# Performance work log

Measured on AMD Instinct MI355X. Metric: run time of the kernel, lower is better.

## Reference

```python
import jax, jax.numpy as jnp
import numpy as np

N_NODES = 50000
N_EDGES = 800000
D = 128
N_LAYERS = 4


def _sage_conv(x, edge_index, Wl, bl, Wr):
    # PyG SAGEConv (mean aggr): out = lin_l(mean_{j in N(i)} x_j) + lin_r(x_i)
    src, dst = edge_index[0], edge_index[1]
    msgs = x[src]                                            # [E, D] gather
    summed = jax.ops.segment_sum(msgs, dst, num_segments=N_NODES)   # [N, D]
    cnt = jax.ops.segment_sum(jnp.ones((msgs.shape[0],), x.dtype), dst,
                              num_segments=N_NODES)
    mean = summed / jnp.maximum(cnt, 1.0)[:, None]           # [N, D]
    return mean @ Wl.T + bl + x @ Wr.T


def setup_inputs() -> dict:
    key = jax.random.key(0)
    ks = jax.random.split(key, 2 + 3 * N_LAYERS)
    x = jax.random.normal(ks[0], (N_NODES, D), dtype=jnp.float32)
    edge_index = jax.random.randint(ks[1], (2, N_EDGES), 0, N_NODES, dtype=jnp.int64)
    inp = {"x": x, "edge_index": edge_index}
    s = 1.0 / np.sqrt(D)
    for i in range(N_LAYERS):
        inp[f"Wl{i}"] = jax.random.uniform(ks[2 + 3 * i], (D, D), jnp.float32, -s, s)
        inp[f"bl{i}"] = jax.random.uniform(ks[3 + 3 * i], (D,), jnp.float32, -s, s)
        inp[f"Wr{i}"] = jax.random.uniform(ks[4 + 3 * i], (D, D), jnp.float32, -s, s)
    return inp


def reference(x, edge_index, Wl0, bl0, Wr0, Wl1, bl1, Wr1, Wl2, bl2, Wr2, Wl3, bl3, Wr3):
    # ReLU only after the first conv, per the original forward.
    h = jax.nn.relu(_sage_conv(x, edge_index, Wl0, bl0, Wr0))
    h = _sage_conv(h, edge_index, Wl1, bl1, Wr1)
    h = _sage_conv(h, edge_index, Wl2, bl2, Wr2)
    h = _sage_conv(h, edge_index, Wl3, bl3, Wr3)
    return h
```

## Files before the change

### kernel.cpp

```cpp
#include <hip/hip_runtime.h>
#include <stdint.h>

#define NN 50000
#define NE 800000
#define CAST_B 6250
#define CVTW_B 512
#define EPB 8192
#define HIST_B 98
#define NBK 196
#define FUSE_B 782

typedef short short8 __attribute__((ext_vector_type(8)));
typedef float f32x4 __attribute__((ext_vector_type(4)));
typedef unsigned int uint;
typedef unsigned short ushort;

__device__ __forceinline__ uint rne_bf16(float f) {
    uint x = __float_as_uint(f);
    return (x + 0x7FFFu + ((x >> 16) & 1u)) >> 16;
}
__device__ __forceinline__ float bf_lo(uint d) { return __uint_as_float(d << 16); }
__device__ __forceinline__ float bf_hi(uint d) { return __uint_as_float(d & 0xFFFF0000u); }

__device__ __forceinline__ int ei_is64(const int* __restrict__ ei) {
    return (ei[1] | ei[3] | ei[5] | ei[7]) == 0;
}

struct Ptrs8 { const float* p[8]; };

__global__ __launch_bounds__(256) void k_prep(
    const float* __restrict__ x, ushort* __restrict__ xbf, Ptrs8 ps,
    ushort* __restrict__ wbf, const int* __restrict__ ei,
    uint* __restrict__ ebuf, int* __restrict__ hcnt) {
    __shared__ int hs[NBK];
    int b = blockIdx.x;
    if (b < CAST_B) {
        int i = b * 256 + threadIdx.x;
        float4 v = ((const float4*)x)[i];
        uint2 o;
        o.x = rne_bf16(v.x) | (rne_bf16(v.y) << 16);
        o.y = rne_bf16(v.z) | (rne_bf16(v.w) << 16);
        ((uint2*)xbf)[i] = o;
    } else if (b < CAST_B + CVTW_B) {
        int idx = (b - CAST_B) * 256 + threadIdx.x;
        int m = idx >> 14;
        int o14 = idx & 16383;
        int k0i = (o14 >> 12) & 3;
        int t = (o14 >> 9) & 7;
        int lane6 = (o14 >> 3) & 63;
        int e = o14 & 7;
        int r = t * 16 + (lane6 & 15);
        int c = k0i * 32 + (lane6 >> 4) * 8 + e;
        wbf[idx] = (ushort)rne_bf16(ps.p[m][r * 128 + c]);
    } else {
        int hb = b - CAST_B - CVTW_B;
        int t = threadIdx.x;
        for (int i = t; i < NBK; i += 256) hs[i] = 0;
        __syncthreads();
        int base = hb * EPB;
        int is64 = ei_is64(ei);
        for (int i = 0; i < EPB; i += 256) {
            int e = base + i + t;
            if (e < NE) {
                int sv = is64 ? ei[2 * e] : ei[e];
                int dv = is64 ? ei[2 * NE + 2 * e] : ei[NE + e];
                ebuf[e] = ((uint)dv << 16) | (uint)sv;
                atomicAdd(&hs[dv >> 8], 1);
            }
        }
        __syncthreads();
        for (int i = t; i < NBK; i += 256) hcnt[hb * NBK + i] = hs[i];
    }
}

__global__ __launch_bounds__(256) void k_scan1(const int* __restrict__ hcnt,
                                               int* __restrict__ hoff,
                                               int* __restrict__ bb,
                                               int* __restrict__ row_ptr) {
    __shared__ int s[256];
    int t = threadIdx.x;
    int tot = 0;
    if (t < NBK)
        for (int b = 0; b < HIST_B; b++) tot += hcnt[b * NBK + t];
    s[t] = tot;
    __syncthreads();
    for (int off = 1; off < 256; off <<= 1) {
        int v = s[t];
        int a = (t >= off) ? s[t - off] : 0;
        __syncthreads();
        s[t] = v + a;
        __syncthreads();
    }
    if (t < NBK) {
        int base = (t == 0) ? 0 : s[t - 1];
        bb[t] = base;
        int run = base;
        for (int b = 0; b < HIST_B; b++) {
            hoff[b * NBK + t] = run;
            run += hcnt[b * NBK + t];
        }
    }
    if (t == 0) { bb[NBK] = NE; row_ptr[NN] = NE; }
}

__global__ __launch_bounds__(256) void k_scatter1(const uint* __restrict__ ebuf,
                                                  const int* __restrict__ hoff,
                                                  uint* __restrict__ ebuf2) {
    __shared__ int pos[NBK];
    int hb = blockIdx.x, t = threadIdx.x;
    for (int i = t; i < NBK; i += 256) pos[i] = hoff[hb * NBK + i];
    __syncthreads();
    int base = hb * EPB;
    for (int i = 0; i < EPB; i += 256) {
        int e = base + i + t;
        if (e < NE) {
            uint pk = ebuf[e];
            int idx = atomicAdd(&pos[pk >> 24], 1);
            ebuf2[idx] = pk;
        }
    }
}

__global__ __launch_bounds__(1024) void k_sort2(const uint* __restrict__ ebuf2,
                                                const int* __restrict__ bb,
                                                int* __restrict__ row_ptr,
                                                ushort* __restrict__ col) {
    __shared__ int hist[256];
    __shared__ int pos[256];
    int k = blockIdx.x, t = threadIdx.x;
    int beg = bb[k], end = bb[k + 1];
    if (t < 256) hist[t] = 0;
    __syncthreads();
    for (int j = beg + t; j < end; j += 1024)
        atomicAdd(&hist[(ebuf2[j] >> 16) & 255], 1);
    __syncthreads();
    for (int off = 1; off < 256; off <<= 1) {
        int v = 0;
        if (t < 256) { v = hist[t]; if (t >= off) v += hist[t - off]; }
        __syncthreads();
        if (t < 256) hist[t] = v;
        __syncthreads();
    }
    if (t < 256) {
        int ex = (t == 0) ? 0 : hist[t - 1];
        pos[t] = beg + ex;
        int node = k * 256 + t;
        if (node < NN) row_ptr[node] = beg + ex;
    }
    __syncthreads();
    for (int j = beg + t; j < end; j += 1024) {
        uint pk = ebuf2[j];
        int idx = atomicAdd(&pos[(pk >> 16) & 255], 1);
        col[idx] = (ushort)(pk & 0xFFFFu);
    }
}

__global__ __launch_bounds__(256) void k_fused(
    const ushort* __restrict__ h, const int* __restrict__ row_ptr,
    const ushort* __restrict__ col, const ushort* __restrict__ Wlb,
    const ushort* __restrict__ Wrb, const float* __restrict__ bias,
    float* __restrict__ outf, ushort* __restrict__ outb, int relu) {
    __shared__ uint smean[64 * 68];
    const int wid = threadIdx.x >> 6;
    const int lane = threadIdx.x & 63;
    const int m0 = blockIdx.x * 64;
    const uint* hp = (const uint*)h;

    for (int ni = 0; ni < 16; ni++) {
        int rl = wid * 16 + ni;
        int node = m0 + rl;
        if (node < NN) {
            int beg = row_ptr[node], end = row_ptr[node + 1];
            float a0 = 0.f, a1 = 0.f;
            for (int b = beg; b < end; b += 64) {
                int n = min(64, end - b);
                int c = (int)col[b + min(lane, n - 1)];
                for (int j0 = 0; j0 < n; j0 += 8) {
#pragma unroll
                    for (int j = 0; j < 8; j++) {
                        int jj = j0 + j;
                        int s = __shfl(c, min(jj, n - 1));
                        uint v = hp[s * 64 + lane];
                        float m = (jj < n) ? 1.f : 0.f;
                        a0 = fmaf(m, bf_lo(v), a0);
                        a1 = fmaf(m, bf_hi(v), a1);
                    }
                }
            }
            float r = 1.0f / (float)max(end - beg, 1);
            smean[rl * 68 + lane] = rne_bf16(a0 * r) | (rne_bf16(a1 * r) << 16);
        } else {
            smean[rl * 68 + lane] = 0;
        }
    }
    __syncthreads();

    const int l15 = lane & 15;
    const int quad = lane >> 4;
    f32x4 acc[8];
#pragma unroll
    for (int t = 0; t < 8; t++) acc[t] = (f32x4){0.f, 0.f, 0.f, 0.f};

    int arow = min(m0 + wid * 16 + l15, NN - 1);
    const ushort* Arh = h + (size_t)arow * 128 + quad * 8;
    const uint* Alds = &smean[(wid * 16 + l15) * 68 + quad * 4];

#pragma unroll
    for (int half = 0; half < 2; half++) {
        const ushort* W = half ? Wrb : Wlb;
#pragma unroll
        for (int k0 = 0; k0 < 128; k0 += 32) {
            short8 a = half ? *(const short8*)(Arh + k0)
                            : *(const short8*)(Alds + (k0 >> 1));
            const ushort* Wk = W + ((k0 >> 5) * 8) * 512 + lane * 8;
#pragma unroll
            for (int t = 0; t < 8; t++) {
                short8 b = *(const short8*)(Wk + t * 512);
                acc[t] = __builtin_amdgcn_mfma_f32_16x16x32_bf16(a, b, acc[t], 0, 0, 0);
            }
        }
    }

    float bb[8];
#pragma unroll
    for (int t = 0; t < 8; t++) bb[t] = bias[t * 16 + l15];

#pragma unroll
    for (int r = 0; r < 4; r++) {
        int row = m0 + wid * 16 + quad * 4 + r;
        if (row < NN) {
#pragma unroll
            for (int t = 0; t < 8; t++) {
                float v = acc[t][r] + bb[t];
                if (relu) v = fmaxf(v, 0.f);
                if (outb) outb[(size_t)row * 128 + t * 16 + l15] = (ushort)rne_bf16(v);
                else outf[(size_t)row * 128 + t * 16 + l15] = v;
            }
        }
    }
}

extern "C" void kernel_launch(void* const* d_in, const int* in_sizes, int n_in,
                              void* d_out, int out_size, void* d_ws, size_t ws_size,
                              hipStream_t stream) {
    const float* x = (const float*)d_in[0];
    const int* ei = (const int*)d_in[1];
    const float* Wl[4] = {(const float*)d_in[2], (const float*)d_in[5],
                          (const float*)d_in[8], (const float*)d_in[11]};
    const float* bl[4] = {(const float*)d_in[3], (const float*)d_in[6],
                          (const float*)d_in[9], (const float*)d_in[12]};
    const float* Wr[4] = {(const float*)d_in[4], (const float*)d_in[7],
                          (const float*)d_in[10], (const float*)d_in[13]};
    float* out = (float*)d_out;

    char* p = (char*)d_ws;
    auto take = [&](size_t bytes) -> char* {
        char* r = p;
        p += (bytes + 255) & ~(size_t)255;
        return r;
    };
    uint* ebuf = (uint*)take((size_t)NE * 4);
    uint* ebuf2 = (uint*)take((size_t)NE * 4);
    int* hcnt = (int*)take((size_t)HIST_B * NBK * 4);
    int* hoff = (int*)take((size_t)HIST_B * NBK * 4);
    int* bb = (int*)take((NBK + 1) * 4);
    int* row_ptr = (int*)take((NN + 1) * 4);
    ushort* col = (ushort*)take((size_t)NE * 2 + 256);
    ushort* xbf = (ushort*)take((size_t)NN * 128 * 2);
    ushort* h1 = (ushort*)take((size_t)NN * 128 * 2);
    ushort* h2 = (ushort*)take((size_t)NN * 128 * 2);
    ushort* wbf = (ushort*)take(8 * 16384 * 2);

    Ptrs8 ps;
    ps.p[0] = Wl[0]; ps.p[1] = Wr[0]; ps.p[2] = Wl[1]; ps.p[3] = Wr[1];
    ps.p[4] = Wl[2]; ps.p[5] = Wr[2]; ps.p[6] = Wl[3]; ps.p[7] = Wr[3];

    k_prep<<<CAST_B + CVTW_B + HIST_B, 256, 0, stream>>>(x, xbf, ps, wbf, ei,
                                                         ebuf, hcnt);
    k_scan1<<<1, 256, 0, stream>>>(hcnt, hoff, bb, row_ptr);
    k_scatter1<<<HIST_B, 256, 0, stream>>>(ebuf, hoff, ebuf2);
    k_sort2<<<NBK, 1024, 0, stream>>>(ebuf2, bb, row_ptr, col);

    const ushort* h = xbf;
    ushort* houts[4] = {h1, h2, h1, nullptr};
    for (int l = 0; l < 4; l++) {
        k_fused<<<FUSE_B, 256, 0, stream>>>(
            h, row_ptr, col, wbf + (size_t)(2 * l) * 16384,
            wbf + (size_t)(2 * l + 1) * 16384, bl[l], out, houts[l],
            l == 0 ? 1 : 0);
        h = houts[l];
    }
}
```

Baseline: 361.7 us.

## Use 16 waves per block in fused SAGE kernel, splitting gather rows and MFMA columns

The fused aggregation+GEMM kernel now runs 1024 threads per block instead of 256. Each wave gathers 4 node rows instead of 16, shortening the serial per-wave gather loop. In the GEMM phase, waves are split into 4 row groups by 4 column groups, each computing 2 output tiles instead of 8. This raises memory-level parallelism for the latency-bound neighbor gather and cuts accumulator registers. The cost is that A fragments are loaded redundantly across column groups, and large blocks may constrain occupancy and scheduling.

```diff
diff --git a/kernel.cpp b/kernel.cpp
--- a/kernel.cpp
+++ b/kernel.cpp
@@ -155,7 +155,7 @@
     }
 }
 
-__global__ __launch_bounds__(256) void k_fused(
+__global__ __launch_bounds__(1024) void k_fused(
     const ushort* __restrict__ h, const int* __restrict__ row_ptr,
     const ushort* __restrict__ col, const ushort* __restrict__ Wlb,
     const ushort* __restrict__ Wrb, const float* __restrict__ bias,
@@ -166,8 +166,9 @@
     const int m0 = blockIdx.x * 64;
     const uint* hp = (const uint*)h;
 
-    for (int ni = 0; ni < 16; ni++) {
-        int rl = wid * 16 + ni;
+#pragma unroll
+    for (int ni = 0; ni < 4; ni++) {
+        int rl = wid * 4 + ni;
         int node = m0 + rl;
         if (node < NN) {
             int beg = row_ptr[node], end = row_ptr[node + 1];
@@ -195,15 +196,17 @@
     }
     __syncthreads();
 
+    const int rowgrp = wid >> 2;
+    const int colgrp = wid & 3;
     const int l15 = lane & 15;
     const int quad = lane >> 4;
-    f32x4 acc[8];
-#pragma unroll
-    for (int t = 0; t < 8; t++) acc[t] = (f32x4){0.f, 0.f, 0.f, 0.f};
-
-    int arow = min(m0 + wid * 16 + l15, NN - 1);
+    f32x4 acc[2];
+    acc[0] = (f32x4){0.f, 0.f, 0.f, 0.f};
+    acc[1] = (f32x4){0.f, 0.f, 0.f, 0.f};
+
+    int arow = min(m0 + rowgrp * 16 + l15, NN - 1);
     const ushort* Arh = h + (size_t)arow * 128 + quad * 8;
-    const uint* Alds = &smean[(wid * 16 + l15) * 68 + quad * 4];
+    const uint* Alds = &smean[(rowgrp * 16 + l15) * 68 + quad * 4];
 
 #pragma unroll
     for (int half = 0; half < 2; half++) {
@@ -214,27 +217,27 @@
                             : *(const short8*)(Alds + (k0 >> 1));
             const ushort* Wk = W + ((k0 >> 5) * 8) * 512 + lane * 8;
 #pragma unroll
-            for (int t = 0; t < 8; t++) {
-                short8 b = *(const short8*)(Wk + t * 512);
-                acc[t] = __builtin_amdgcn_mfma_f32_16x16x32_bf16(a, b, acc[t], 0, 0, 0);
-            }
-        }
-    }
-
-    float bb[8];
-#pragma unroll
-    for (int t = 0; t < 8; t++) bb[t] = bias[t * 16 + l15];
+            for (int tt = 0; tt < 2; tt++) {
+                short8 b = *(const short8*)(Wk + (size_t)(colgrp * 2 + tt) * 512);
+                acc[tt] = __builtin_amdgcn_mfma_f32_16x16x32_bf16(a, b, acc[tt], 0, 0, 0);
+            }
+        }
+    }
+
+    float bb2[2] = {bias[(colgrp * 2 + 0) * 16 + l15],
+                    bias[(colgrp * 2 + 1) * 16 + l15]};
 
 #pragma unroll
     for (int r = 0; r < 4; r++) {
-        int row = m0 + wid * 16 + quad * 4 + r;
+        int row = m0 + rowgrp * 16 + quad * 4 + r;
         if (row < NN) {
 #pragma unroll
-            for (int t = 0; t < 8; t++) {
-                float v = acc[t][r] + bb[t];
+            for (int tt = 0; tt < 2; tt++) {
+                int cidx = (colgrp * 2 + tt) * 16 + l15;
+                float v = acc[tt][r] + bb2[tt];
                 if (relu) v = fmaxf(v, 0.f);
-                if (outb) outb[(size_t)row * 128 + t * 16 + l15] = (ushort)rne_bf16(v);
-                else outf[(size_t)row * 128 + t * 16 + l15] = v;
+                if (outb) outb[(size_t)row * 128 + cidx] = (ushort)rne_bf16(v);
+                else outf[(size_t)row * 128 + cidx] = v;
             }
         }
     }
@@ -284,7 +287,7 @@
     const ushort* h = xbf;
     ushort* houts[4] = {h1, h2, h1, nullptr};
     for (int l = 0; l < 4; l++) {
-        k_fused<<<FUSE_B, 256, 0, stream>>>(
+        k_fused<<<FUSE_B, 1024, 0, stream>>>(
             h, row_ptr, col, wbf + (size_t)(2 * l) * 16384,
             wbf + (size_t)(2 * l + 1) * 16384, bl[l], out, houts[l],
             l == 0 ? 1 : 0);
```

Measured after the change: 360.3 us. Within noise of the previous version (-0.4%).
